# Kernel tuning notes

Hardware: AMD Instinct MI355X
Metric: run time of the kernel (lower is better)

Reference implementation:

```python
import jax, jax.numpy as jnp
import numpy as np

G, N, D = 32, 2048, 128          # graphs, nodes per graph, feature dim
E_PER = 16384                     # edges per graph (avg degree 8)
E = G * E_PER
RATIO = 0.5
K = int(np.ceil(RATIO * N))       # nodes kept per graph = 1024


def setup_inputs() -> dict:
    key = jax.random.key(0)
    ks = jax.random.split(key, 8)
    x = jax.random.normal(ks[0], (G * N, D), dtype=jnp.float32)
    # random intra-graph edges, then offset into the global node index space
    src = jax.random.randint(ks[1], (G, E_PER), 0, N)
    dst = jax.random.randint(ks[2], (G, E_PER), 0, N)
    off = (jnp.arange(G) * N)[:, None]
    edge_index = jnp.stack([(src + off).reshape(-1), (dst + off).reshape(-1)]).astype(jnp.int32)
    batch = jnp.repeat(jnp.arange(G, dtype=jnp.int32), N)
    s = 1.0 / np.sqrt(D)
    w_rel = jax.random.normal(ks[3], (D,), dtype=jnp.float32) * s   # GraphConv lin_rel weight (out=1)
    b_rel = jnp.zeros((), dtype=jnp.float32)                         # GraphConv bias
    w_root = jax.random.normal(ks[4], (D,), dtype=jnp.float32) * s  # GraphConv lin_root (no bias)
    w_lin = jax.random.normal(ks[5], (D,), dtype=jnp.float32) * s   # nn.Linear(in_dim, 1)
    b_lin = jnp.zeros((), dtype=jnp.float32)
    return {"x": x, "edge_index": edge_index, "batch": batch,
            "w_rel": w_rel, "b_rel": b_rel, "w_root": w_root,
            "w_lin": w_lin, "b_lin": b_lin}


def reference(x, edge_index, batch, w_rel, b_rel, w_root, w_lin, b_lin):
    n_nodes = x.shape[0]
    src, dst = edge_index[0], edge_index[1]

    # score1 = GraphConv(x, edge_index): W_root x_i + W_rel * sum_{j->i} x_j + b
    agg = jax.ops.segment_sum(x[src], dst, num_segments=n_nodes)     # [n_nodes, D]
    score1 = agg @ w_rel + b_rel + x @ w_root                         # [n_nodes]
    # score2 = Linear(x)
    score2 = x @ w_lin + b_lin                                        # [n_nodes]
    # elementwise max over the two scores (torch.max over cat dim=1)
    score = jnp.maximum(score1, score2)

    # per-graph topk: batch is block-sorted with equal graph sizes
    _, idx = jax.lax.top_k(score.reshape(G, N), K)                    # [G, K] intra-graph idx
    perm = (idx + (jnp.arange(G) * N)[:, None]).reshape(-1)           # [G*K] global idx

    x_out = x[perm] * jnp.tanh(score[perm])[:, None]                  # [G*K, D]

    # filter_adj: keep edges whose endpoints both survive, re-index nodes.
    # Output edge count is data-dependent; we return a fixed-size reindexed
    # edge_index plus a validity mask (invalid edges set to 0).
    new_idx = jnp.full((n_nodes,), -1, dtype=edge_index.dtype)
    new_idx = new_idx.at[perm].set(jnp.arange(perm.shape[0], dtype=edge_index.dtype))
    ns, nd = new_idx[src], new_idx[dst]
    edge_mask = (ns >= 0) & (nd >= 0)
    new_edge_index = jnp.where(edge_mask, jnp.stack([ns, nd]), 0)

    new_batch = batch[perm]
    return (x_out, new_edge_index, edge_mask, new_batch)
```

## Files before the change

### kernel.cpp

```cpp
#include <hip/hip_runtime.h>
#include <hip/hip_bf16.h>

#define G_     32
#define N_     2048
#define D_     128
#define K_     1024
#define EPER_  16384

__global__ __launch_bounds__(256) void node_dots(
    const float* __restrict__ x,
    const float* __restrict__ w_rel,
    const float* __restrict__ w_root,
    const float* __restrict__ w_lin,
    const float* __restrict__ b_rel_p,
    const float* __restrict__ b_lin_p,
    float* __restrict__ p,
    float* __restrict__ base,
    float* __restrict__ s2,
    int n_nodes)
{
    int wave = (blockIdx.x * 256 + threadIdx.x) >> 6;
    int lane = threadIdx.x & 63;
    int node = wave * 2 + (lane >> 5);
    int c    = lane & 31;
    if (node >= n_nodes) return;

    float4 xv = ((const float4*)(x + (size_t)node * D_))[c];
    float4 wr = ((const float4*)w_rel)[c];
    float4 wo = ((const float4*)w_root)[c];
    float4 wl = ((const float4*)w_lin)[c];

    float pr = xv.x * wr.x + xv.y * wr.y + xv.z * wr.z + xv.w * wr.w;
    float po = xv.x * wo.x + xv.y * wo.y + xv.z * wo.z + xv.w * wo.w;
    float pl = xv.x * wl.x + xv.y * wl.y + xv.z * wl.z + xv.w * wl.w;

    #pragma unroll
    for (int off = 16; off; off >>= 1) {
        pr += __shfl_xor(pr, off);
        po += __shfl_xor(po, off);
        pl += __shfl_xor(pl, off);
    }
    if (c == 0) {
        p[node]    = pr;
        base[node] = po + b_rel_p[0];
        s2[node]   = pl + b_lin_p[0];
    }
}

__global__ __launch_bounds__(1024) void agg_score(
    const int* __restrict__ src, const int* __restrict__ dst,
    const float* __restrict__ p,
    const float* __restrict__ base, const float* __restrict__ s2,
    float* __restrict__ score)
{
    __shared__ float agg[N_];
    int g = blockIdx.x;
    for (int i = threadIdx.x; i < N_; i += 1024) agg[i] = 0.0f;
    __syncthreads();

    const int* gsrc = src + (size_t)g * EPER_;
    const int* gdst = dst + (size_t)g * EPER_;
    const float* gp = p + (size_t)g * N_;
    #pragma unroll 4
    for (int e = threadIdx.x; e < EPER_; e += 1024) {
        int s_ = gsrc[e] & (N_ - 1);
        int d_ = gdst[e] & (N_ - 1);
        atomicAdd(&agg[d_], gp[s_]);
    }
    __syncthreads();

    for (int i = threadIdx.x; i < N_; i += 1024) {
        int node = g * N_ + i;
        score[node] = fmaxf(base[node] + agg[i], s2[node]);
    }
}

__global__ __launch_bounds__(1024) void topk_rank(
    const float* __restrict__ score,
    int* __restrict__ new_idx, int* __restrict__ perm)
{
    __shared__ unsigned long long keys[N_];
    __shared__ int cnt[256];
    int g   = blockIdx.x >> 3;
    int sub = blockIdx.x & 7;
    const float* gs = score + (size_t)g * N_;

    for (int i = threadIdx.x; i < N_; i += 1024) {
        unsigned u = __float_as_uint(gs[i]);
        u ^= ((int)u < 0) ? 0xFFFFFFFFu : 0x80000000u;
        keys[i] = ((unsigned long long)u << 32) | (unsigned)(N_ - 1 - i);
    }
    if (threadIdx.x < 256) cnt[threadIdx.x] = 0;
    __syncthreads();

    int il = threadIdx.x & 255;
    int jq = threadIdx.x >> 8;
    int mi = sub * 256 + il;
    unsigned long long ki = keys[mi];

    const ulonglong2* k2 = (const ulonglong2*)keys;
    int c = 0;
    #pragma unroll 4
    for (int h = jq * 256; h < jq * 256 + 256; ++h) {
        ulonglong2 kk = k2[h];
        c += (kk.x > ki) + (kk.y > ki);
    }
    atomicAdd(&cnt[il], c);
    __syncthreads();

    if (threadIdx.x < 256) {
        int node = g * N_ + sub * 256 + threadIdx.x;
        int rank = cnt[threadIdx.x];
        if (rank < K_) {
            int pos = g * K_ + rank;
            perm[pos] = node;
            new_idx[node] = pos;
        } else {
            new_idx[node] = -1;
        }
    }
}

__global__ __launch_bounds__(256) void gather_scale(
    const float* __restrict__ x, const float* __restrict__ score,
    const int* __restrict__ perm,
    float* __restrict__ out_x, float* __restrict__ out_b)
{
    int t   = blockIdx.x * 256 + threadIdx.x;
    int row = t >> 5;
    int c   = t & 31;
    int node = perm[row];
    float tz = tanhf(score[node]);
    float4 xv = ((const float4*)(x + (size_t)node * D_))[c];
    float4 v  = make_float4(xv.x * tz, xv.y * tz, xv.z * tz, xv.w * tz);
    ((float4*)(out_x + (size_t)row * D_))[c] = v;
    if (c == 0) out_b[row] = (float)(node >> 11);
}

__global__ __launch_bounds__(256) void edge_out_kernel(
    const int* __restrict__ src, const int* __restrict__ dst,
    const int* __restrict__ new_idx,
    float* __restrict__ out_e0,
    float* __restrict__ out_e1,
    float* __restrict__ out_m, int E)
{
    int e = blockIdx.x * 256 + threadIdx.x;
    if (e >= E) return;
    int ns = new_idx[src[e]];
    int nd = new_idx[dst[e]];
    bool m = (ns >= 0) && (nd >= 0);
    out_e0[e] = m ? (float)ns : 0.0f;
    out_e1[e] = m ? (float)nd : 0.0f;
    out_m[e]  = m ? 1.0f : 0.0f;
}

extern "C" void kernel_launch(void* const* d_in, const int* in_sizes, int n_in,
                              void* d_out, int out_size, void* d_ws, size_t ws_size,
                              hipStream_t stream)
{
    const float* x      = (const float*)d_in[0];
    const int*   ei     = (const int*)d_in[1];
    const float* w_rel  = (const float*)d_in[3];
    const float* b_rel  = (const float*)d_in[4];
    const float* w_root = (const float*)d_in[5];
    const float* w_lin  = (const float*)d_in[6];
    const float* b_lin  = (const float*)d_in[7];
    float* out = (float*)d_out;

    const int n_nodes = in_sizes[0] / D_;
    const int E       = in_sizes[1] / 2;
    const int* src = ei;
    const int* dst = ei + E;

    float* p      = (float*)d_ws;
    float* base   = p + n_nodes;
    float* s2     = base + n_nodes;
    float* score  = s2 + n_nodes;
    int*   new_idx = (int*)(score + n_nodes);
    int*   perm    = new_idx + n_nodes;

    const size_t offEI = (size_t)G_ * K_ * D_;
    const size_t offM  = offEI + 2 * (size_t)E;
    const size_t offB  = offM + (size_t)E;

    node_dots<<<n_nodes / 2 / 4, 256, 0, stream>>>(
        x, w_rel, w_root, w_lin, b_rel, b_lin, p, base, s2, n_nodes);
    agg_score<<<G_, 1024, 0, stream>>>(src, dst, p, base, s2, score);
    topk_rank<<<G_ * 8, 1024, 0, stream>>>(score, new_idx, perm);
    gather_scale<<<(G_ * K_ * 32) / 256, 256, 0, stream>>>(
        x, score, perm, out, out + offB);
    edge_out_kernel<<<(E + 255) / 256, 256, 0, stream>>>(
        src, dst, new_idx, out + offEI, out + offEI + E, out + offM, E);
}
```

Baseline: 139.0 us.

## Split edge aggregation and top-k ranking into more parallel blocks with global partials

```diff
diff --git a/kernel.cpp b/kernel.cpp
--- a/kernel.cpp
+++ b/kernel.cpp
@@ -47,77 +47,79 @@
     }
 }
 
-__global__ __launch_bounds__(1024) void agg_score(
+__global__ __launch_bounds__(1024) void agg_partial(
     const int* __restrict__ src, const int* __restrict__ dst,
-    const float* __restrict__ p,
+    const float* __restrict__ p, float* __restrict__ part)
+{
+    __shared__ float agg[N_];
+    int g = blockIdx.x >> 3;
+    int s = blockIdx.x & 7;
+    agg[threadIdx.x]        = 0.0f;
+    agg[threadIdx.x + 1024] = 0.0f;
+    __syncthreads();
+
+    int e0 = g * EPER_ + s * 2048 + threadIdx.x;
+    int e1 = e0 + 1024;
+    const float* gp = p + (size_t)g * N_;
+    atomicAdd(&agg[dst[e0] & (N_ - 1)], gp[src[e0] & (N_ - 1)]);
+    atomicAdd(&agg[dst[e1] & (N_ - 1)], gp[src[e1] & (N_ - 1)]);
+    __syncthreads();
+
+    float* op = part + ((size_t)g * 8 + s) * N_;
+    op[threadIdx.x]        = agg[threadIdx.x];
+    op[threadIdx.x + 1024] = agg[threadIdx.x + 1024];
+}
+
+__global__ __launch_bounds__(1024) void score_key(
+    const float* __restrict__ part,
     const float* __restrict__ base, const float* __restrict__ s2,
-    float* __restrict__ score)
-{
-    __shared__ float agg[N_];
-    int g = blockIdx.x;
-    for (int i = threadIdx.x; i < N_; i += 1024) agg[i] = 0.0f;
-    __syncthreads();
-
-    const int* gsrc = src + (size_t)g * EPER_;
-    const int* gdst = dst + (size_t)g * EPER_;
-    const float* gp = p + (size_t)g * N_;
-    #pragma unroll 4
-    for (int e = threadIdx.x; e < EPER_; e += 1024) {
-        int s_ = gsrc[e] & (N_ - 1);
-        int d_ = gdst[e] & (N_ - 1);
-        atomicAdd(&agg[d_], gp[s_]);
-    }
-    __syncthreads();
-
-    for (int i = threadIdx.x; i < N_; i += 1024) {
-        int node = g * N_ + i;
-        score[node] = fmaxf(base[node] + agg[i], s2[node]);
-    }
-}
-
-__global__ __launch_bounds__(1024) void topk_rank(
-    const float* __restrict__ score,
+    float* __restrict__ score, unsigned long long* __restrict__ keys)
+{
+    int node = blockIdx.x * 1024 + threadIdx.x;
+    int g = node >> 11;
+    int i = node & (N_ - 1);
+    const float* pp = part + (size_t)g * 8 * N_ + i;
+    float a = 0.0f;
+    #pragma unroll
+    for (int s = 0; s < 8; ++s) a += pp[(size_t)s * N_];
+    float sc = fmaxf(base[node] + a, s2[node]);
+    score[node] = sc;
+    unsigned u = __float_as_uint(sc);
+    u ^= ((int)u < 0) ? 0xFFFFFFFFu : 0x80000000u;
+    keys[node] = ((unsigned long long)u << 32) | (unsigned)(N_ - 1 - i);
+}
+
+__global__ __launch_bounds__(1024) void topk_cnt(
+    const unsigned long long* __restrict__ keys, int* __restrict__ cpart)
+{
+    int g  = blockIdx.x >> 3;
+    int ib = (blockIdx.x >> 2) & 1;
+    int jh = blockIdx.x & 3;
+    const unsigned long long* gk = keys + (size_t)g * N_;
+    int i = ib * 1024 + threadIdx.x;
+    unsigned long long ki = gk[i];
+    const unsigned long long* jk = gk + jh * 512;
+    int c = 0;
+    #pragma unroll 8
+    for (int j = 0; j < 512; ++j) c += (jk[j] > ki) ? 1 : 0;
+    cpart[((size_t)g * 4 + jh) * N_ + i] = c;
+}
+
+__global__ __launch_bounds__(256) void topk_merge(
+    const int* __restrict__ cpart,
     int* __restrict__ new_idx, int* __restrict__ perm)
 {
-    __shared__ unsigned long long keys[N_];
-    __shared__ int cnt[256];
-    int g   = blockIdx.x >> 3;
-    int sub = blockIdx.x & 7;
-    const float* gs = score + (size_t)g * N_;
-
-    for (int i = threadIdx.x; i < N_; i += 1024) {
-        unsigned u = __float_as_uint(gs[i]);
-        u ^= ((int)u < 0) ? 0xFFFFFFFFu : 0x80000000u;
-        keys[i] = ((unsigned long long)u << 32) | (unsigned)(N_ - 1 - i);
-    }
-    if (threadIdx.x < 256) cnt[threadIdx.x] = 0;
-    __syncthreads();
-
-    int il = threadIdx.x & 255;
-    int jq = threadIdx.x >> 8;
-    int mi = sub * 256 + il;
-    unsigned long long ki = keys[mi];
-
-    const ulonglong2* k2 = (const ulonglong2*)keys;
-    int c = 0;
-    #pragma unroll 4
-    for (int h = jq * 256; h < jq * 256 + 256; ++h) {
-        ulonglong2 kk = k2[h];
-        c += (kk.x > ki) + (kk.y > ki);
-    }
-    atomicAdd(&cnt[il], c);
-    __syncthreads();
-
-    if (threadIdx.x < 256) {
-        int node = g * N_ + sub * 256 + threadIdx.x;
-        int rank = cnt[threadIdx.x];
-        if (rank < K_) {
-            int pos = g * K_ + rank;
-            perm[pos] = node;
-            new_idx[node] = pos;
-        } else {
-            new_idx[node] = -1;
-        }
+    int node = blockIdx.x * 256 + threadIdx.x;
+    int g = node >> 11;
+    int i = node & (N_ - 1);
+    const int* cp = cpart + (size_t)g * 4 * N_ + i;
+    int rank = cp[0] + cp[N_] + cp[2 * N_] + cp[3 * N_];
+    if (rank < K_) {
+        int pos = g * K_ + rank;
+        perm[pos] = node;
+        new_idx[node] = pos;
+    } else {
+        new_idx[node] = -1;
     }
 }
 
@@ -172,21 +174,26 @@
     const int* src = ei;
     const int* dst = ei + E;
 
-    float* p      = (float*)d_ws;
-    float* base   = p + n_nodes;
-    float* s2     = base + n_nodes;
-    float* score  = s2 + n_nodes;
-    int*   new_idx = (int*)(score + n_nodes);
+    unsigned long long* keys = (unsigned long long*)d_ws;
+    float* p     = (float*)(keys + n_nodes);
+    float* base  = p + n_nodes;
+    float* s2    = base + n_nodes;
+    float* score = s2 + n_nodes;
+    float* part  = score + n_nodes;
+    int*   cpart = (int*)(part + (size_t)G_ * 8 * N_);
+    int*   new_idx = cpart + (size_t)G_ * 4 * N_;
     int*   perm    = new_idx + n_nodes;
 
     const size_t offEI = (size_t)G_ * K_ * D_;
     const size_t offM  = offEI + 2 * (size_t)E;
     const size_t offB  = offM + (size_t)E;
 
-    node_dots<<<n_nodes / 2 / 4, 256, 0, stream>>>(
+    node_dots<<<n_nodes / 8, 256, 0, stream>>>(
         x, w_rel, w_root, w_lin, b_rel, b_lin, p, base, s2, n_nodes);
-    agg_score<<<G_, 1024, 0, stream>>>(src, dst, p, base, s2, score);
-    topk_rank<<<G_ * 8, 1024, 0, stream>>>(score, new_idx, perm);
+    agg_partial<<<G_ * 8, 1024, 0, stream>>>(src, dst, p, part);
+    score_key<<<n_nodes / 1024, 1024, 0, stream>>>(part, base, s2, score, keys);
+    topk_cnt<<<G_ * 8, 1024, 0, stream>>>(keys, cpart);
+    topk_merge<<<n_nodes / 256, 256, 0, stream>>>(cpart, new_idx, perm);
     gather_scale<<<(G_ * K_ * 32) / 256, 256, 0, stream>>>(
         x, score, perm, out, out + offB);
     edge_out_kernel<<<(E + 255) / 256, 256, 0, stream>>>(
```

Result: faster. 132.2 us (-4.9%).
